# Kernel tuning notes

Hardware: AMD Instinct MI355X
Metric: run time of the kernel (lower is better)

The kernel has to match this reference:

```python
import jax, jax.numpy as jnp
import numpy as np

B, S, HID, H, DH = 4, 1024, 1024, 16, 64
MAX_REL = 16
SCALE = 1.0 / (DH ** 0.5)


def _rel_bias(emb, seq_len):
    # Shaw-style relative position bias: emb is [2*MAX_REL+1, DH]
    pos = jnp.arange(seq_len)
    dist = jnp.clip(pos[None, :] - pos[:, None], -MAX_REL, MAX_REL) + MAX_REL
    return emb[dist]  # [S, S, DH]


def setup_inputs() -> dict:
    key = jax.random.key(0)
    ks = jax.random.split(key, 14)
    n = jax.random.normal
    w = 0.02
    return {
        "query": n(ks[0], (B, S, HID), dtype=jnp.float32),
        "key": n(ks[1], (B, S, HID), dtype=jnp.float32),
        "value": n(ks[2], (B, S, HID), dtype=jnp.float32),
        # per-head projection weights stacked over heads
        "Wq": n(ks[3], (H, HID, DH), dtype=jnp.float32) * w,
        "bq": n(ks[4], (H, DH), dtype=jnp.float32) * w,
        "Wk": n(ks[5], (H, HID, DH), dtype=jnp.float32) * w,
        "bk": n(ks[6], (H, DH), dtype=jnp.float32) * w,
        "Wv": n(ks[7], (H, HID, DH), dtype=jnp.float32) * w,
        "bv": n(ks[8], (H, DH), dtype=jnp.float32) * w,
        # relative-position embedding tables (shared across heads)
        "rel_k_emb": n(ks[9], (2 * MAX_REL + 1, DH), dtype=jnp.float32) * w,
        "rel_v_emb": n(ks[10], (2 * MAX_REL + 1, DH), dtype=jnp.float32) * w,
        # output projection fc: Linear(hidden, hidden)
        "fc_W": n(ks[11], (HID, HID), dtype=jnp.float32) * w,
        "fc_b": n(ks[12], (HID,), dtype=jnp.float32) * w,
    }


def reference(query, key, value, Wq, bq, Wk, bk, Wv, bv, rel_k_emb, rel_v_emb, fc_W, fc_b):
    # per-head projections, all heads batched: [B, H, S, DH]
    q = jnp.einsum('bsd,hde->bhse', query, Wq) + bq[None, :, None, :]
    k = jnp.einsum('bsd,hde->bhse', key, Wk) + bk[None, :, None, :]
    v = jnp.einsum('bsd,hde->bhse', value, Wv) + bv[None, :, None, :]

    k_bias = _rel_bias(rel_k_emb, S)  # [S, S, DH]
    v_bias = _rel_bias(rel_v_emb, S)  # [S, S, DH]

    # scores: QK^T plus relative-position key bias term
    scores = jnp.einsum('bhqe,bhke->bhqk', q, k)
    scores = scores + jnp.einsum('bhqe,qke->bhqk', q, k_bias)
    attn = jax.nn.softmax(scores * SCALE, axis=-1)  # [B, H, S, S]

    # values: A V plus relative-position value bias term
    out = jnp.einsum('bhqk,bhke->bhqe', attn, v)
    out = out + jnp.einsum('bhqk,qke->bhqe', attn, v_bias)

    # concat heads -> [B, S, HID], then fc
    out = out.transpose(0, 2, 1, 3).reshape(B, S, HID)
    return out @ fc_W.T + fc_b
```

## Files before the change

kernel.cpp:

```cpp
#include <hip/hip_runtime.h>
#include <stdint.h>

#define B_ 4
#define S_ 1024
#define HID_ 1024
#define H_ 16
#define DH_ 64
#define NDIST 33
#define SCALE_ 0.125f

typedef unsigned short u16;
typedef __attribute__((ext_vector_type(8))) short short8;
typedef __attribute__((ext_vector_type(4))) float floatx4;

static __device__ __forceinline__ float bf2f(u16 u) {
  union { unsigned int i; float f; } v; v.i = ((unsigned int)u) << 16; return v.f;
}
static __device__ __forceinline__ u16 f2bf(float x) {
  union { float f; unsigned int i; } v; v.f = x;
  return (u16)((v.i + 0x7FFFu + ((v.i >> 16) & 1u)) >> 16);
}
static __device__ __forceinline__ floatx4 mfma_bf16(short8 a, short8 b, floatx4 c) {
  return __builtin_amdgcn_mfma_f32_16x16x32_bf16(a, b, c, 0, 0, 0);
}

#define OFF_BQ   0
#define OFF_BK   1024
#define OFF_BV   2048
#define OFF_RELK 3072
#define OFF_RELV 5184
#define OFF_FCW  7296
#define OFF_FCB  1055872
#define CONV_TOT 1056896

struct SrcPtrs { const void* p[7]; };

__global__ __launch_bounds__(256) void detect_kernel(const u16* __restrict__ q,
                                                     int* __restrict__ flag) {
  __shared__ float red[256];
  float m = 0.f;
  for (int i = threadIdx.x; i < 8192; i += 256) {
    float v = fabsf(bf2f(q[2 * i]));
    m = fmaxf(m, (v < 1e30f) ? v : 1e20f);
  }
  red[threadIdx.x] = m;
  __syncthreads();
  for (int s = 128; s > 0; s >>= 1) {
    if (threadIdx.x < (unsigned)s) red[threadIdx.x] = fmaxf(red[threadIdx.x], red[threadIdx.x + s]);
    __syncthreads();
  }
  if (threadIdx.x == 0) *flag = (red[0] > 1e4f) ? 1 : 0;
}

__global__ __launch_bounds__(256) void convert_kernel(SrcPtrs srcs,
                                                      const int* __restrict__ flag,
                                                      u16* __restrict__ dst) {
  constexpr int segsz[7] = {1024,1024,1024,2112,2112,1048576,1024};
  constexpr int cumE[7]  = {OFF_BQ,OFF_BK,OFF_BV,OFF_RELK,OFF_RELV,OFF_FCW,OFF_FCB};
  constexpr int cumB[8]  = {0,1,2,3,6,9,1033,1034};
  const int bid = blockIdx.x;
  int t = 0;
  #pragma unroll
  for (int i = 1; i < 7; ++i) if (bid >= cumB[i]) t = i;
  const int chunk = (bid - cumB[t]) * 1024 + threadIdx.x * 4;
  if (chunk >= segsz[t]) return;
  __align__(8) u16 o[4];
  if (*flag) {
    const float* s = (const float*)srcs.p[t];
    float4 v = *(const float4*)(s + chunk);
    o[0] = f2bf(v.x); o[1] = f2bf(v.y); o[2] = f2bf(v.z); o[3] = f2bf(v.w);
  } else {
    const u16* s = (const u16*)srcs.p[t];
    *(uint2*)o = *(const uint2*)(s + chunk);
  }
  *(uint2*)(dst + cumE[t] + chunk) = *(const uint2*)o;
}

__global__ __launch_bounds__(256) void wtrans_kernel(
    const void* __restrict__ Wq, const void* __restrict__ Wk, const void* __restrict__ Wv,
    const int* __restrict__ flag, u16* __restrict__ wt)
{
  const int dt = blockIdx.x, h = blockIdx.y, z = blockIdx.z;
  const void* W = (z == 0) ? Wq : (z == 1) ? Wk : Wv;
  const int tid = threadIdx.x;
  const int isf = *flag;
  __shared__ __align__(16) u16 t_l[64 * 72];

  #pragma unroll
  for (int i = 0; i < 2; ++i) {
    int g = tid + 256 * i;
    int d = g & 63, e8 = (g >> 6) * 8;
    size_t off = ((size_t)h * HID_ + dt * 64 + d) * DH_ + e8;
    __align__(16) u16 tmp[8];
    if (isf) {
      const float* Wf = (const float*)W + off;
      float4 v0 = *(const float4*)Wf;
      float4 v1 = *(const float4*)(Wf + 4);
      tmp[0]=f2bf(v0.x); tmp[1]=f2bf(v0.y); tmp[2]=f2bf(v0.z); tmp[3]=f2bf(v0.w);
      tmp[4]=f2bf(v1.x); tmp[5]=f2bf(v1.y); tmp[6]=f2bf(v1.z); tmp[7]=f2bf(v1.w);
    } else {
      *(uint4*)tmp = *(const uint4*)((const u16*)W + off);
    }
    #pragma unroll
    for (int j = 0; j < 8; ++j) {
      int e = e8 + j;
      t_l[e * 72 + (((d >> 3) ^ (e & 7)) << 3) + (d & 7)] = tmp[j];
    }
  }
  __syncthreads();
  {
    int e = tid >> 2, c0 = (tid & 3) * 2;
    u16* dst = wt + ((size_t)(z * H_ + h) * DH_ + e) * HID_ + dt * 64;
    uint4 x0 = *(const uint4*)(t_l + e * 72 + (((c0    ) ^ (e & 7)) << 3));
    uint4 x1 = *(const uint4*)(t_l + e * 72 + (((c0 + 1) ^ (e & 7)) << 3));
    *(uint4*)(dst + c0 * 8)     = x0;
    *(uint4*)(dst + c0 * 8 + 8) = x1;
  }
}

__global__ __launch_bounds__(256) void proj_kernel(
    const void* __restrict__ qin, const void* __restrict__ kin, const void* __restrict__ vin,
    const u16* __restrict__ wt, const u16* __restrict__ conv,
    const int* __restrict__ flag,
    u16* __restrict__ qo, u16* __restrict__ ko, u16* __restrict__ vo)
{
  const int z = blockIdx.z;
  const void* A   = (z == 0) ? qin : (z == 1) ? kin : vin;
  const u16* Wz   = wt + (size_t)z * (H_ * DH_ * HID_);
  const u16* bias = conv + ((z == 0) ? OFF_BQ : (z == 1) ? OFF_BK : OFF_BV);
  u16*       O    = (z == 0) ? qo : (z == 1) ? ko : vo;
  const int rt = blockIdx.x, ct = blockIdx.y;
  const int tid = threadIdx.x, lane = tid & 63, w = tid >> 6, quad = lane >> 4, l16 = lane & 15;
  const int isf = *flag;

  __shared__ __align__(16) u16 a_l[128 * 32];
  __shared__ __align__(16) u16 b_l[128 * 32];

  floatx4 acc[4][4];
  #pragma unroll
  for (int i = 0; i < 4; ++i)
    #pragma unroll
    for (int j = 0; j < 4; ++j) acc[i][j] = (floatx4){0.f,0.f,0.f,0.f};

  const int mq = (w & 1) * 64, nq = (w >> 1) * 64;

  for (int kk = 0; kk < 32; ++kk) {
    __syncthreads();
    #pragma unroll
    for (int i = 0; i < 2; ++i) {
      int idx = tid + 256 * i;
      int row = idx >> 2, c8 = (idx & 3) * 8;
      if (isf) {
        const float* Af = (const float*)A + (size_t)(rt * 128 + row) * HID_ + kk * 32 + c8;
        float4 v0 = *(const float4*)Af;
        float4 v1 = *(const float4*)(Af + 4);
        __align__(16) u16 tmp[8] = {f2bf(v0.x),f2bf(v0.y),f2bf(v0.z),f2bf(v0.w),
                                    f2bf(v1.x),f2bf(v1.y),f2bf(v1.z),f2bf(v1.w)};
        *(uint4*)(a_l + row * 32 + c8) = *(const uint4*)tmp;
      } else {
        *(uint4*)(a_l + row * 32 + c8) =
            *(const uint4*)((const u16*)A + (size_t)(rt * 128 + row) * HID_ + kk * 32 + c8);
      }
      *(uint4*)(b_l + row * 32 + c8) =
          *(const uint4*)(Wz + (size_t)(ct * 128 + row) * HID_ + kk * 32 + c8);
    }
    __syncthreads();
    short8 af[4], bfr[4];
    #pragma unroll
    for (int i = 0; i < 4; ++i) {
      af[i]  = *(const short8*)(a_l + (mq + i * 16 + l16) * 32 + quad * 8);
      bfr[i] = *(const short8*)(b_l + (nq + i * 16 + l16) * 32 + quad * 8);
    }
    #pragma unroll
    for (int i = 0; i < 4; ++i)
      #pragma unroll
      for (int j = 0; j < 4; ++j)
        acc[i][j] = mfma_bf16(af[i], bfr[j], acc[i][j]);
  }

  #pragma unroll
  for (int j = 0; j < 4; ++j) {
    int col = ct * 128 + nq + j * 16 + l16;
    int hh = col >> 6, e = col & 63;
    float bb = bf2f(bias[hh * 64 + e]);
    #pragma unroll
    for (int i = 0; i < 4; ++i) {
      #pragma unroll
      for (int r = 0; r < 4; ++r) {
        int m = rt * 128 + mq + i * 16 + quad * 4 + r;
        int bidx = m >> 10, srow = m & 1023;
        O[(((size_t)(bidx * H_ + hh)) * S_ + srow) * DH_ + e] = f2bf(acc[i][j][r] + bb);
      }
    }
  }
}

__global__ __launch_bounds__(256, 4) void attn_kernel(
    const u16* __restrict__ Q, const u16* __restrict__ K, const u16* __restrict__ V,
    const u16* __restrict__ conv, u16* __restrict__ Ox)
{
  const int bid = blockIdx.x + 16 * (blockIdx.y + 16 * blockIdx.z);
  const int nid = (bid & 7) * 128 + (bid >> 3);
  const int qt = nid & 15, h = (nid >> 4) & 15, b = nid >> 8;

  const int tid = threadIdx.x;
  const int lane = tid & 63, w = tid >> 6, quad = lane >> 4, l16 = lane & 15;
  const size_t base = ((size_t)(b * H_ + h)) * S_ * DH_;

  __shared__ __align__(16) char smem[40320];
  u16*   p_l    = (u16*)(smem);
  u16*   q_l    = p_l;
  u16*   k_l    = (u16*)(smem + 9216);
  u16*   vt_l   = (u16*)(smem + 18432);
  u16*   rq_l   = (u16*)(smem + 27648);
  float* bucket = (float*)(smem + 31872);
  u16*   rkb    = (u16*)(smem + 31872);

  #pragma unroll
  for (int i = 0; i < 2; ++i) {
    int idx = tid + 256 * i;
    int row = idx >> 3, c8 = (idx & 7) * 8;
    *(uint4*)(q_l + row * 72 + c8) =
        *(const uint4*)(Q + base + (size_t)(qt * 64 + row) * DH_ + c8);
  }
  const u16* relk = conv + OFF_RELK;
  for (int idx = tid; idx < 48 * 8; idx += 256) {
    int row = idx >> 3, c8 = (idx & 7) * 8;
    uint4 v = make_uint4(0, 0, 0, 0);
    if (row < NDIST) v = *(const uint4*)(relk + row * 64 + c8);
    *(uint4*)(rkb + row * 72 + c8) = v;
  }
  __syncthreads();

  const int m0 = w * 16;
  short8 qa0 = *(const short8*)(q_l + (m0 + l16) * 72 + quad * 8);
  short8 qa1 = *(const short8*)(q_l + (m0 + l16) * 72 + 32 + quad * 8);

  #pragma unroll
  for (int t3 = 0; t3 < 3; ++t3) {
    floatx4 c = {0.f,0.f,0.f,0.f};
    c = mfma_bf16(qa0, *(const short8*)(rkb + (t3 * 16 + l16) * 72 + quad * 8), c);
    c = mfma_bf16(qa1, *(const short8*)(rkb + (t3 * 16 + l16) * 72 + 32 + quad * 8), c);
    int d = t3 * 16 + l16;
    if (d < NDIST) {
      #pragma unroll
      for (int r = 0; r < 4; ++r) rq_l[(m0 + quad * 4 + r) * 33 + d] = f2bf(c[r]);
    }
  }
  __syncthreads();
  for (int idx = tid; idx < 64 * 33; idx += 256) bucket[idx] = 0.f;

  floatx4 o[4], oi = {0.f,0.f,0.f,0.f};
  #pragma unroll
  for (int t = 0; t < 4; ++t) o[t] = (floatx4){0.f,0.f,0.f,0.f};

  for (int kt = 0; kt < 16; ++kt) {
    __syncthreads();
    #pragma unroll
    for (int i = 0; i < 2; ++i) {
      int idx = tid + 256 * i;
      int row = idx >> 3, c8 = (idx & 7) * 8;
      *(uint4*)(k_l + row * 72 + c8) =
          *(const uint4*)(K + base + (size_t)(kt * 64 + row) * DH_ + c8);
    }
    {
      int kcol = lane;
      #pragma unroll
      for (int ph = 0; ph < 2; ++ph) {
        int e8 = w * 16 + ph * 8;
        uint4 vv = *(const uint4*)(V + base + (size_t)(kt * 64 + kcol) * DH_ + e8);
        const u16* t8 = (const u16*)&vv;
        #pragma unroll
        for (int j = 0; j < 8; ++j) {
          vt_l[(e8 + j) * 72 + kcol] = t8[j];
        }
      }
    }
    __syncthreads();

    const int dkt = kt - qt;
    const bool near = (dkt >= -1) && (dkt <= 1);

    #pragma unroll
    for (int t = 0; t < 4; ++t) {
      floatx4 s = {0.f,0.f,0.f,0.f};
      s = mfma_bf16(qa0, *(const short8*)(k_l + (t * 16 + l16) * 72 + quad * 8), s);
      s = mfma_bf16(qa1, *(const short8*)(k_l + (t * 16 + l16) * 72 + 32 + quad * 8), s);
      int kcol = t * 16 + l16;
      #pragma unroll
      for (int r = 0; r < 4; ++r) {
        int m = m0 + quad * 4 + r;
        int delta = (kt * 64 + kcol) - (qt * 64 + m);
        int dist = (delta < -16 ? -16 : (delta > 16 ? 16 : delta)) + 16;
        float logit = (s[r] + bf2f(rq_l[m * 33 + dist])) * SCALE_;
        u16 pu = f2bf(__expf(fminf(logit, 30.f)));
        p_l[m * 72 + kcol] = pu;
        if (near) {
          float pv = bf2f(pu);
          float vhi = (dist == 32) ? pv : 0.f;
          float vlo = (dist == 0) ? pv : 0.f;
          #pragma unroll
          for (int off2 = 1; off2 < 16; off2 <<= 1) {
            vhi += __shfl_xor(vhi, off2, 16);
            vlo += __shfl_xor(vlo, off2, 16);
          }
          if (l16 == 0) {
            if (vhi != 0.f) atomicAdd(&bucket[m * 33 + 32], vhi);
            if (vlo != 0.f) atomicAdd(&bucket[m * 33 + 0], vlo);
          }
          if (dist > 0 && dist < 32) atomicAdd(&bucket[m * 33 + dist], pv);
        }
      }
    }

    u16 iv = ((l16 == 0 && dkt <= -2) || (l16 == 1 && dkt >= 2)) ? (u16)0x3F80 : (u16)0;
    short8 ib;
    #pragma unroll
    for (int j = 0; j < 8; ++j) ib[j] = (short)iv;
    short8 pa0 = *(const short8*)(p_l + (m0 + l16) * 72 + quad * 8);
    short8 pa1 = *(const short8*)(p_l + (m0 + l16) * 72 + 32 + quad * 8);
    oi = mfma_bf16(pa0, ib, oi);
    oi = mfma_bf16(pa1, ib, oi);
    #pragma unroll
    for (int t = 0; t < 4; ++t) {
      int e = t * 16 + l16;
      short8 vb0 = *(const short8*)(vt_l + e * 72 + quad * 8);
      short8 vb1 = *(const short8*)(vt_l + e * 72 + 32 + quad * 8);
      o[t] = mfma_bf16(pa0, vb0, o[t]);
      o[t] = mfma_bf16(pa1, vb1, o[t]);
    }
  }

  __syncthreads();
  if (l16 == 0) {
    #pragma unroll
    for (int r = 0; r < 4; ++r) bucket[(m0 + quad * 4 + r) * 33 + 0] += oi[r];
  } else if (l16 == 1) {
    #pragma unroll
    for (int r = 0; r < 4; ++r) bucket[(m0 + quad * 4 + r) * 33 + 32] += oi[r];
  }
  __syncthreads();

  u16* rvT = k_l;
  u16* Bf  = p_l;
  for (int idx = tid; idx < 576; idx += 256) {
    ((uint4*)rvT)[idx] = make_uint4(0, 0, 0, 0);
    ((uint4*)Bf)[idx]  = make_uint4(0, 0, 0, 0);
  }
  __syncthreads();
  const u16* relv = conv + OFF_RELV;
  for (int idx = tid; idx < NDIST * 64; idx += 256) {
    int d = idx >> 6, e = idx & 63;
    rvT[e * 72 + d] = relv[idx];
  }
  for (int idx = tid; idx < 64 * NDIST; idx += 256) {
    int m = idx / NDIST, d = idx - m * NDIST;
    Bf[m * 72 + d] = f2bf(bucket[m * 33 + d]);
  }
  __syncthreads();

  short8 ba0 = *(const short8*)(Bf + (m0 + l16) * 72 + quad * 8);
  short8 ba1 = *(const short8*)(Bf + (m0 + l16) * 72 + 32 + quad * 8);
  #pragma unroll
  for (int t = 0; t < 4; ++t) {
    short8 rb0 = *(const short8*)(rvT + (t * 16 + l16) * 72 + quad * 8);
    short8 rb1 = *(const short8*)(rvT + (t * 16 + l16) * 72 + 32 + quad * 8);
    o[t] = mfma_bf16(ba0, rb0, o[t]);
    o[t] = mfma_bf16(ba1, rb1, o[t]);
  }

  float rl[4];
  #pragma unroll
  for (int r = 0; r < 4; ++r) {
    int m = m0 + quad * 4 + r;
    float s = 0.f;
    #pragma unroll
    for (int d = 0; d < NDIST; ++d) s += bucket[m * 33 + d];
    rl[r] = 1.f / s;
  }

  #pragma unroll
  for (int t = 0; t < 4; ++t) {
    int e = t * 16 + l16;
    #pragma unroll
    for (int r = 0; r < 4; ++r) {
      int srow = qt * 64 + m0 + quad * 4 + r;
      Ox[((size_t)(b * S_ + srow)) * HID_ + h * 64 + e] = f2bf(o[t][r] * rl[r]);
    }
  }
}

__global__ __launch_bounds__(256) void fc_kernel(
    const u16* __restrict__ X, const u16* __restrict__ conv,
    const int* __restrict__ flag, void* __restrict__ outv)
{
  const u16* Wf  = conv + OFF_FCW;
  const u16* bfc = conv + OFF_FCB;
  const int rt = blockIdx.x, ct = blockIdx.y;
  const int tid = threadIdx.x, lane = tid & 63, w = tid >> 6, quad = lane >> 4, l16 = lane & 15;
  const int isf = *flag;

  __shared__ __align__(16) u16 a_l[128 * 32];
  __shared__ __align__(16) u16 b_l[128 * 32];

  floatx4 acc[4][4];
  #pragma unroll
  for (int i = 0; i < 4; ++i)
    #pragma unroll
    for (int j = 0; j < 4; ++j) acc[i][j] = (floatx4){0.f,0.f,0.f,0.f};

  const int mq = (w & 1) * 64, nq = (w >> 1) * 64;

  for (int kk = 0; kk < 32; ++kk) {
    __syncthreads();
    #pragma unroll
    for (int i = 0; i < 2; ++i) {
      int idx = tid + 256 * i;
      int row = idx >> 2, c8 = (idx & 3) * 8;
      *(uint4*)(a_l + row * 32 + c8) =
          *(const uint4*)(X + (size_t)(rt * 128 + row) * HID_ + kk * 32 + c8);
      *(uint4*)(b_l + row * 32 + c8) =
          *(const uint4*)(Wf + (size_t)(ct * 128 + row) * HID_ + kk * 32 + c8);
    }
    __syncthreads();
    short8 af[4], bfr[4];
    #pragma unroll
    for (int i = 0; i < 4; ++i) {
      af[i]  = *(const short8*)(a_l + (mq + i * 16 + l16) * 32 + quad * 8);
      bfr[i] = *(const short8*)(b_l + (nq + i * 16 + l16) * 32 + quad * 8);
    }
    #pragma unroll
    for (int i = 0; i < 4; ++i)
      #pragma unroll
      for (int j = 0; j < 4; ++j)
        acc[i][j] = mfma_bf16(af[i], bfr[j], acc[i][j]);
  }

  #pragma unroll
  for (int j = 0; j < 4; ++j) {
    int col = ct * 128 + nq + j * 16 + l16;
    float bb = bf2f(bfc[col]);
    #pragma unroll
    for (int i = 0; i < 4; ++i) {
      #pragma unroll
      for (int r = 0; r < 4; ++r) {
        int m = rt * 128 + mq + i * 16 + quad * 4 + r;
        float val = acc[i][j][r] + bb;
        size_t idx = (size_t)m * HID_ + col;
        if (isf) ((float*)outv)[idx] = val;
        else     ((u16*)outv)[idx]   = f2bf(val);
      }
    }
  }
}

extern "C" void kernel_launch(void* const* d_in, const int* in_sizes, int n_in,
                              void* d_out, int out_size, void* d_ws, size_t ws_size,
                              hipStream_t stream) {
  int* flag = (int*)d_ws;
  u16* conv = (u16*)((char*)d_ws + 16);
  u16* wt   = conv + CONV_TOT;
  u16* qw   = wt + 3145728;
  u16* kw   = qw + 4194304;
  u16* vw   = kw + 4194304;
  u16* xw   = vw + 4194304;

  detect_kernel<<<1, 256, 0, stream>>>((const u16*)d_in[0], flag);

  SrcPtrs sp;
  sp.p[0] = d_in[4];  sp.p[1] = d_in[6];  sp.p[2] = d_in[8];
  sp.p[3] = d_in[9];  sp.p[4] = d_in[10]; sp.p[5] = d_in[11]; sp.p[6] = d_in[12];
  convert_kernel<<<1034, 256, 0, stream>>>(sp, flag, conv);

  wtrans_kernel<<<dim3(16, 16, 3), 256, 0, stream>>>(d_in[3], d_in[5], d_in[7], flag, wt);
  proj_kernel<<<dim3(32, 8, 3), 256, 0, stream>>>(d_in[0], d_in[1], d_in[2],
                                                  wt, conv, flag, qw, kw, vw);
  attn_kernel<<<dim3(16, 16, 4), 256, 0, stream>>>(qw, kw, vw, conv, xw);
  fc_kernel<<<dim3(32, 8), 256, 0, stream>>>(xw, conv, flag, (u16*)d_out);
}
```

Measured before the change: 320.6 us.

## Use direct global-to-LDS loads in GEMMs and fast path for far-tile logits

Replaces register-staged global-to-shared copies in the projection and output GEMMs with global_load_lds direct loads, where each wave writes a contiguous 64-element LDS chunk at a wave-uniform base. In the attention kernel, tiles far from the diagonal now take a separate path that uses a precomputed per-row clipped bias (distance 0 or 32) held in registers, skipping the per-element distance computation and LDS bias lookup. The direct-load path depends on the builtin's wave-uniform LDS addressing matching the old row-major layout, and the attention change adds register pressure and a divergent branch.

```diff
diff --git a/kernel.cpp b/kernel.cpp
--- a/kernel.cpp
+++ b/kernel.cpp
@@ -22,6 +22,11 @@
 }
 static __device__ __forceinline__ floatx4 mfma_bf16(short8 a, short8 b, floatx4 c) {
   return __builtin_amdgcn_mfma_f32_16x16x32_bf16(a, b, c, 0, 0, 0);
+}
+static __device__ __forceinline__ void gload_lds16(const void* g, void* l) {
+  __builtin_amdgcn_global_load_lds(
+      (const __attribute__((address_space(1))) unsigned int*)g,
+      (__attribute__((address_space(3))) unsigned int*)l, 16, 0, 0);
 }
 
 #define OFF_BQ   0
@@ -161,8 +166,8 @@
         *(uint4*)(a_l + row * 32 + c8) =
             *(const uint4*)((const u16*)A + (size_t)(rt * 128 + row) * HID_ + kk * 32 + c8);
       }
-      *(uint4*)(b_l + row * 32 + c8) =
-          *(const uint4*)(Wz + (size_t)(ct * 128 + row) * HID_ + kk * 32 + c8);
+      gload_lds16(Wz + (size_t)(ct * 128 + row) * HID_ + kk * 32 + c8,
+                  b_l + ((size_t)(w * 64 + i * 256)) * 8);
     }
     __syncthreads();
     short8 af[4], bfr[4];
@@ -236,16 +241,25 @@
   short8 qa0 = *(const short8*)(q_l + (m0 + l16) * 72 + quad * 8);
   short8 qa1 = *(const short8*)(q_l + (m0 + l16) * 72 + 32 + quad * 8);
 
+  floatx4 c_d0 = {0.f,0.f,0.f,0.f}, c_d32 = {0.f,0.f,0.f,0.f};
   #pragma unroll
   for (int t3 = 0; t3 < 3; ++t3) {
     floatx4 c = {0.f,0.f,0.f,0.f};
     c = mfma_bf16(qa0, *(const short8*)(rkb + (t3 * 16 + l16) * 72 + quad * 8), c);
     c = mfma_bf16(qa1, *(const short8*)(rkb + (t3 * 16 + l16) * 72 + 32 + quad * 8), c);
+    if (t3 == 0) c_d0 = c;
+    if (t3 == 2) c_d32 = c;
     int d = t3 * 16 + l16;
     if (d < NDIST) {
       #pragma unroll
       for (int r = 0; r < 4; ++r) rq_l[(m0 + quad * 4 + r) * 33 + d] = f2bf(c[r]);
     }
+  }
+  float rqs_lo[4], rqs_hi[4];
+  #pragma unroll
+  for (int r = 0; r < 4; ++r) {
+    rqs_lo[r] = bf2f(f2bf(__shfl(c_d0[r],  lane & 48, 64))) * SCALE_;
+    rqs_hi[r] = bf2f(f2bf(__shfl(c_d32[r], lane & 48, 64))) * SCALE_;
   }
   __syncthreads();
   for (int idx = tid; idx < 64 * 33; idx += 256) bucket[idx] = 0.f;
@@ -287,15 +301,15 @@
       s = mfma_bf16(qa0, *(const short8*)(k_l + (t * 16 + l16) * 72 + quad * 8), s);
       s = mfma_bf16(qa1, *(const short8*)(k_l + (t * 16 + l16) * 72 + 32 + quad * 8), s);
       int kcol = t * 16 + l16;
-      #pragma unroll
-      for (int r = 0; r < 4; ++r) {
-        int m = m0 + quad * 4 + r;
-        int delta = (kt * 64 + kcol) - (qt * 64 + m);
-        int dist = (delta < -16 ? -16 : (delta > 16 ? 16 : delta)) + 16;
-        float logit = (s[r] + bf2f(rq_l[m * 33 + dist])) * SCALE_;
-        u16 pu = f2bf(__expf(fminf(logit, 30.f)));
-        p_l[m * 72 + kcol] = pu;
-        if (near) {
+      if (near) {
+        #pragma unroll
+        for (int r = 0; r < 4; ++r) {
+          int m = m0 + quad * 4 + r;
+          int delta = (kt * 64 + kcol) - (qt * 64 + m);
+          int dist = (delta < -16 ? -16 : (delta > 16 ? 16 : delta)) + 16;
+          float logit = (s[r] + bf2f(rq_l[m * 33 + dist])) * SCALE_;
+          u16 pu = f2bf(__expf(fminf(logit, 30.f)));
+          p_l[m * 72 + kcol] = pu;
           float pv = bf2f(pu);
           float vhi = (dist == 32) ? pv : 0.f;
           float vlo = (dist == 0) ? pv : 0.f;
@@ -310,6 +324,14 @@
           }
           if (dist > 0 && dist < 32) atomicAdd(&bucket[m * 33 + dist], pv);
         }
+      } else {
+        #pragma unroll
+        for (int r = 0; r < 4; ++r) {
+          int m = m0 + quad * 4 + r;
+          float logit = fmaf(s[r], SCALE_, (dkt < 0) ? rqs_lo[r] : rqs_hi[r]);
+          u16 pu = f2bf(__expf(fminf(logit, 30.f)));
+          p_l[m * 72 + kcol] = pu;
+        }
       }
     }
 
@@ -417,10 +439,10 @@
     for (int i = 0; i < 2; ++i) {
       int idx = tid + 256 * i;
       int row = idx >> 2, c8 = (idx & 3) * 8;
-      *(uint4*)(a_l + row * 32 + c8) =
-          *(const uint4*)(X + (size_t)(rt * 128 + row) * HID_ + kk * 32 + c8);
-      *(uint4*)(b_l + row * 32 + c8) =
-          *(const uint4*)(Wf + (size_t)(ct * 128 + row) * HID_ + kk * 32 + c8);
+      gload_lds16(X + (size_t)(rt * 128 + row) * HID_ + kk * 32 + c8,
+                  a_l + ((size_t)(w * 64 + i * 256)) * 8);
+      gload_lds16(Wf + (size_t)(ct * 128 + row) * HID_ + kk * 32 + c8,
+                  b_l + ((size_t)(w * 64 + i * 256)) * 8);
     }
     __syncthreads();
     short8 af[4], bfr[4];
```

New measurement: 310.9 us. 3.0% less time.
